# Performance work log

Measured on AMD Instinct MI355X. Metric: run time of the kernel, lower is better.

## Reference

```python
import jax, jax.numpy as jnp
import numpy as np

SCALE_FACTOR = 1.0
VIS_MAX = 1024


def setup_inputs() -> dict:
    key = jax.random.key(0)
    kq, kk, kv = jax.random.split(key, 3)
    B, C, H, W = 4, 256, 64, 64
    Q = jax.random.normal(kq, (B, C, H, W), dtype=jnp.float32)
    K = jax.random.normal(kk, (B, C, H, W), dtype=jnp.float32)
    V = jax.random.normal(kv, (B, C, H, W), dtype=jnp.float32)
    return {"Q": Q, "K": K, "V": V}


def reference(Q, K, V):
    # Q,K: [B,C,H,W] -> flatten spatial dims to HW
    B, C, H, W = Q.shape
    HW = H * W
    Q_flat = Q.reshape(B, C, HW).transpose(0, 2, 1)  # [B, HW, C]
    K_flat = K.reshape(B, C, HW)                      # [B, C, HW]
    # Full scaled score matrix [B, HW, HW]; argmax over keys reproduces the
    # chunked running-max/argmax (strict '>' update keeps first max, matching
    # jnp.argmax tie-breaking).
    S = jnp.einsum('bqc,bck->bqk', Q_flat, K_flat) * SCALE_FACTOR
    H_idx = jnp.argmax(S, axis=2).astype(jnp.int64)   # [B, HW]
    vis = min(VIS_MAX, HW)
    S_vis = S[:, :vis, :vis]                          # [B, vis, vis]
    return S_vis, H_idx
```

## Files before the change

### kernel.cpp

```cpp
#include <hip/hip_runtime.h>
#include <stdint.h>

#define B_   4
#define C_   256
#define HW_  4096
#define VIS_ 1024
#define KE_  768

using half8   = __attribute__((ext_vector_type(8))) _Float16;
using floatx4 = __attribute__((ext_vector_type(4))) float;

__device__ __forceinline__ unsigned mapf(float v) {
    unsigned u = __float_as_uint(v);
    return (u & 0x80000000u) ? ~u : (u | 0x80000000u);
}

__global__ void init_ws_kernel(unsigned long long* ws, int n) {
    int i = blockIdx.x * blockDim.x + threadIdx.x;
    if (i < n) ws[i] = 0ull;
}

__global__ void finalize_kernel(const unsigned long long* __restrict__ ws,
                                float* __restrict__ out1, int n) {
    int i = blockIdx.x * blockDim.x + threadIdx.x;
    if (i < n) {
        unsigned kinv = (unsigned)(ws[i] & 0xFFFFFFFFull);
        out1[i] = (float)(HW_ - 1 - (int)kinv);
    }
}


__global__ __launch_bounds__(256) void split_transpose_kernel(
    const float* __restrict__ Q, const float* __restrict__ K,
    _Float16* __restrict__ Aexp, _Float16* __restrict__ Bexp)
{
    __shared__ float tile[64][65];
    const int hw0 = blockIdx.x * 64;
    const int c0  = blockIdx.y * 64;
    const int z = blockIdx.z, b = z >> 1, which = z & 1;
    const float* src = (which ? K : Q) + (size_t)b * C_ * HW_;
    _Float16* dst = (which ? Bexp : Aexp) + (size_t)b * HW_ * KE_;
    const int t = threadIdx.x;

    #pragma unroll
    for (int i = 0; i < 4; ++i) {
        int c  = (t >> 4) + i * 16;
        int hw = (t & 15) * 4;
        float4 v = *(const float4*)(src + (size_t)(c0 + c) * HW_ + hw0 + hw);
        tile[c][hw] = v.x; tile[c][hw+1] = v.y; tile[c][hw+2] = v.z; tile[c][hw+3] = v.w;
    }
    __syncthreads();

    #pragma unroll
    for (int i = 0; i < 2; ++i) {
        int id  = t + i * 256;
        int row = id >> 3;
        int c8  = (id & 7) * 8;
        half8 h8, l8;
        #pragma unroll
        for (int j = 0; j < 8; ++j) {
            float v = tile[c8 + j][row];
            _Float16 h = (_Float16)v;
            h8[j] = h;
            l8[j] = (_Float16)(v - (float)h);
        }
        _Float16* base = dst + (size_t)(hw0 + row) * KE_ + c0 + c8;
        *(half8*)(base + 0 * C_) = h8;
        *(half8*)(base + 1 * C_) = which ? l8 : h8;
        *(half8*)(base + 2 * C_) = which ? h8 : l8;
    }
}

__device__ __forceinline__ void gl2lds16(const _Float16* g, _Float16* l) {
    __builtin_amdgcn_global_load_lds(
        (const __attribute__((address_space(1))) void*)g,
        (__attribute__((address_space(3))) void*)l, 16, 0, 0);
}

__global__ __launch_bounds__(256, 2) void gemm_mfma_kernel(
    const _Float16* __restrict__ Aexp, const _Float16* __restrict__ Bexp,
    float* __restrict__ out0, unsigned long long* __restrict__ keys)
{
    __shared__ __align__(16) _Float16 Al[128 * 32];
    __shared__ __align__(16) _Float16 Bl[128 * 32];
    __shared__ unsigned long long red2[128][2];

    const int t    = threadIdx.x;
    const int lane = t & 63;
    const int wave = t >> 6;
    const int quad = lane >> 4;
    const int s    = lane & 15;
    const int wm   = (wave >> 1) * 64;
    const int wn   = (wave & 1) * 64;
    const int kt = blockIdx.x, qt = blockIdx.y, b = blockIdx.z;

    const _Float16* Ab = Aexp + (size_t)b * HW_ * KE_ + (size_t)(qt * 128) * KE_;
    const _Float16* Bb = Bexp + (size_t)b * HW_ * KE_ + (size_t)(kt * 128) * KE_;

    const int ca = t, cb = t + 256;
    const int ra = ca >> 2, oa = (ca & 3) * 8;
    const int rb = cb >> 2, ob = (cb & 3) * 8;

    floatx4 acc[4][4] = {};

    for (int it = 0; it < KE_ / 32; ++it) {
        const int k0 = it * 32;
        gl2lds16(Ab + (size_t)ra * KE_ + k0 + oa, Al + ca * 8);
        gl2lds16(Ab + (size_t)rb * KE_ + k0 + ob, Al + cb * 8);
        gl2lds16(Bb + (size_t)ra * KE_ + k0 + oa, Bl + ca * 8);
        gl2lds16(Bb + (size_t)rb * KE_ + k0 + ob, Bl + cb * 8);
        __syncthreads();

        half8 a[4], bf[4];
        #pragma unroll
        for (int mi = 0; mi < 4; ++mi)
            a[mi] = *(half8*)(Al + (wm + mi * 16 + s) * 32 + quad * 8);
        #pragma unroll
        for (int ni = 0; ni < 4; ++ni)
            bf[ni] = *(half8*)(Bl + (wn + ni * 16 + s) * 32 + quad * 8);
        #pragma unroll
        for (int mi = 0; mi < 4; ++mi)
            #pragma unroll
            for (int ni = 0; ni < 4; ++ni)
                acc[mi][ni] = __builtin_amdgcn_mfma_f32_16x16x32_f16(a[mi], bf[ni], acc[mi][ni], 0, 0, 0);
        __syncthreads();
    }

    if (qt < 8 && kt < 8) {
        #pragma unroll
        for (int mi = 0; mi < 4; ++mi)
            #pragma unroll
            for (int r = 0; r < 4; ++r) {
                int grow = qt * 128 + wm + mi * 16 + quad * 4 + r;
                float* orow = out0 + ((size_t)b * VIS_ + grow) * VIS_ + kt * 128;
                #pragma unroll
                for (int ni = 0; ni < 4; ++ni)
                    orow[wn + ni * 16 + s] = acc[mi][ni][r];
            }
    }

    #pragma unroll
    for (int mi = 0; mi < 4; ++mi) {
        #pragma unroll
        for (int r = 0; r < 4; ++r) {
            float best = acc[mi][0][r];
            int bcol = wn + s;
            #pragma unroll
            for (int ni = 1; ni < 4; ++ni) {
                float v = acc[mi][ni][r];
                if (v > best) { best = v; bcol = wn + ni * 16 + s; }
            }
            int gcol = kt * 128 + bcol;
            unsigned long long key = ((unsigned long long)mapf(best) << 32)
                                   | (unsigned)(HW_ - 1 - gcol);
            #pragma unroll
            for (int m = 1; m < 16; m <<= 1) {
                unsigned long long o = __shfl_xor(key, m, 64);
                if (o > key) key = o;
            }
            if (s == 0) red2[wm + mi * 16 + quad * 4 + r][wave & 1] = key;
        }
    }
    __syncthreads();
    if (t < 128) {
        unsigned long long k0v = red2[t][0], k1v = red2[t][1];
        unsigned long long kk = k0v > k1v ? k0v : k1v;
        atomicMax(&keys[(size_t)b * HW_ + qt * 128 + t], kk);
    }
}

#define BT   64
#define BK   32
#define LDP  68

__global__ __launch_bounds__(256) void gemm_argmax_kernel(
    const float* __restrict__ Q, const float* __restrict__ K,
    float* __restrict__ out0, unsigned long long* __restrict__ ws)
{
    __shared__ float As[BK][LDP];
    __shared__ float Bs[BK][LDP];
    __shared__ unsigned long long red[BT][17];

    const int t  = threadIdx.x;
    const int tx = t & 15;
    const int ty = t >> 4;
    const int k0 = blockIdx.x * BT;
    const int q0 = blockIdx.y * BT;
    const int b  = blockIdx.z;

    const float* Qb = Q + (size_t)b * C_ * HW_;
    const float* Kb = K + (size_t)b * C_ * HW_;

    float acc[4][4] = {{0.f},{0.f},{0.f},{0.f}};

    for (int c0 = 0; c0 < C_; c0 += BK) {
        #pragma unroll
        for (int i = 0; i < 2; ++i) {
            int idx = i * 256 + t;
            int row = idx >> 4;
            int col = (idx & 15) * 4;
            const float4 a  = *(const float4*)(Qb + (size_t)(c0 + row) * HW_ + q0 + col);
            const float4 bv = *(const float4*)(Kb + (size_t)(c0 + row) * HW_ + k0 + col);
            *(float4*)(&As[row][col]) = a;
            *(float4*)(&Bs[row][col]) = bv;
        }
        __syncthreads();
        #pragma unroll
        for (int cc = 0; cc < BK; ++cc) {
            const float4 av = *(const float4*)(&As[cc][ty * 4]);
            const float4 bv = *(const float4*)(&Bs[cc][tx * 4]);
            const float a_[4] = {av.x, av.y, av.z, av.w};
            const float b_[4] = {bv.x, bv.y, bv.z, bv.w};
            #pragma unroll
            for (int i = 0; i < 4; ++i)
                #pragma unroll
                for (int j = 0; j < 4; ++j)
                    acc[i][j] = fmaf(a_[i], b_[j], acc[i][j]);
        }
        __syncthreads();
    }

    if (q0 < VIS_ && k0 < VIS_) {
        #pragma unroll
        for (int i = 0; i < 4; ++i) {
            float4 v = make_float4(acc[i][0], acc[i][1], acc[i][2], acc[i][3]);
            size_t off = (size_t)b * VIS_ * VIS_ + (size_t)(q0 + ty * 4 + i) * VIS_ + (k0 + tx * 4);
            *(float4*)(out0 + off) = v;
        }
    }

    #pragma unroll
    for (int i = 0; i < 4; ++i) {
        float best = acc[i][0];
        int   bj   = 0;
        #pragma unroll
        for (int j = 1; j < 4; ++j)
            if (acc[i][j] > best) { best = acc[i][j]; bj = j; }
        int kidx = k0 + tx * 4 + bj;
        unsigned long long key = ((unsigned long long)mapf(best) << 32)
                               | (unsigned)(HW_ - 1 - kidx);
        red[ty * 4 + i][tx] = key;
    }
    __syncthreads();
    if (t < BT) {
        unsigned long long best = red[t][0];
        #pragma unroll
        for (int j = 1; j < 16; ++j) {
            unsigned long long v = red[t][j];
            if (v > best) best = v;
        }
        atomicMax(&ws[(size_t)b * HW_ + q0 + t], best);
    }
}

extern "C" void kernel_launch(void* const* d_in, const int* in_sizes, int n_in,
                              void* d_out, int out_size, void* d_ws, size_t ws_size,
                              hipStream_t stream) {
    const float* Q = (const float*)d_in[0];
    const float* K = (const float*)d_in[1];
    float* out0 = (float*)d_out;
    float* out1 = out0 + (size_t)B_ * VIS_ * VIS_;

    unsigned long long* keys = (unsigned long long*)d_ws;
    const size_t keys_bytes = (size_t)B_ * HW_ * 8;
    const size_t exp_elems  = (size_t)B_ * HW_ * KE_;
    const size_t need = keys_bytes + 2 * exp_elems * sizeof(_Float16);

    const int n = B_ * HW_;
    init_ws_kernel<<<(n + 255) / 256, 256, 0, stream>>>(keys, n);

    if (ws_size >= need) {
        _Float16* Aexp = (_Float16*)((char*)d_ws + keys_bytes);
        _Float16* Bexp = Aexp + exp_elems;
        split_transpose_kernel<<<dim3(HW_ / 64, C_ / 64, 2 * B_), 256, 0, stream>>>(Q, K, Aexp, Bexp);
        gemm_mfma_kernel<<<dim3(HW_ / 128, HW_ / 128, B_), 256, 0, stream>>>(Aexp, Bexp, out0, keys);
    } else {
        gemm_argmax_kernel<<<dim3(HW_ / BT, HW_ / BT, B_), 256, 0, stream>>>(Q, K, out0, keys);
    }

    finalize_kernel<<<(n + 255) / 256, 256, 0, stream>>>(keys, out1, n);
}
```

Before: 233.8 us.

## Switch to 32x32x16 MFMA, dedupe hi/lo split storage, fuse key init

The GEMM now issues 32x32x16 f16 MFMAs on a 2x2 accumulator tile per wave instead of 16x16x32 on a 4x4 tile. The split-precision buffers store hi and lo halves once (512 instead of 768 columns), and the three-phase K loop picks hi/lo offsets by phase. This cuts workspace writes and footprint, and the larger MFMA needs fewer LDS reads per FLOP. The separate zero-init kernel is folded into the transpose kernel, saving one launch. The output and argmax epilogue are remapped to the 32x32 accumulator layout, which risks indexing mistakes.

```diff
diff --git a/kernel.cpp b/kernel.cpp
--- a/kernel.cpp
+++ b/kernel.cpp
@@ -5,10 +5,10 @@
 #define C_   256
 #define HW_  4096
 #define VIS_ 1024
-#define KE_  768
-
-using half8   = __attribute__((ext_vector_type(8))) _Float16;
-using floatx4 = __attribute__((ext_vector_type(4))) float;
+#define KS_  512
+
+using half8    = __attribute__((ext_vector_type(8))) _Float16;
+using floatx16 = __attribute__((ext_vector_type(16))) float;
 
 __device__ __forceinline__ unsigned mapf(float v) {
     unsigned u = __float_as_uint(v);
@@ -32,15 +32,19 @@
 
 __global__ __launch_bounds__(256) void split_transpose_kernel(
     const float* __restrict__ Q, const float* __restrict__ K,
-    _Float16* __restrict__ Aexp, _Float16* __restrict__ Bexp)
+    _Float16* __restrict__ Aexp, _Float16* __restrict__ Bexp,
+    unsigned long long* __restrict__ keys)
 {
     __shared__ float tile[64][65];
     const int hw0 = blockIdx.x * 64;
     const int c0  = blockIdx.y * 64;
     const int z = blockIdx.z, b = z >> 1, which = z & 1;
     const float* src = (which ? K : Q) + (size_t)b * C_ * HW_;
-    _Float16* dst = (which ? Bexp : Aexp) + (size_t)b * HW_ * KE_;
+    _Float16* dst = (which ? Bexp : Aexp) + (size_t)b * HW_ * KS_;
     const int t = threadIdx.x;
+
+    if (blockIdx.y == 0 && blockIdx.z == 0)
+        keys[blockIdx.x * 256 + t] = 0ull;
 
     #pragma unroll
     for (int i = 0; i < 4; ++i) {
@@ -64,10 +68,9 @@
             h8[j] = h;
             l8[j] = (_Float16)(v - (float)h);
         }
-        _Float16* base = dst + (size_t)(hw0 + row) * KE_ + c0 + c8;
-        *(half8*)(base + 0 * C_) = h8;
-        *(half8*)(base + 1 * C_) = which ? l8 : h8;
-        *(half8*)(base + 2 * C_) = which ? h8 : l8;
+        _Float16* base = dst + (size_t)(hw0 + row) * KS_ + c0 + c8;
+        *(half8*)(base)       = h8;
+        *(half8*)(base + 256) = l8;
     }
 }
 
@@ -88,77 +91,83 @@
     const int t    = threadIdx.x;
     const int lane = t & 63;
     const int wave = t >> 6;
-    const int quad = lane >> 4;
-    const int s    = lane & 15;
+    const int l31  = lane & 31;
+    const int g    = lane >> 5;
     const int wm   = (wave >> 1) * 64;
     const int wn   = (wave & 1) * 64;
     const int kt = blockIdx.x, qt = blockIdx.y, b = blockIdx.z;
 
-    const _Float16* Ab = Aexp + (size_t)b * HW_ * KE_ + (size_t)(qt * 128) * KE_;
-    const _Float16* Bb = Bexp + (size_t)b * HW_ * KE_ + (size_t)(kt * 128) * KE_;
+    const _Float16* Ab = Aexp + (size_t)b * HW_ * KS_ + (size_t)(qt * 128) * KS_;
+    const _Float16* Bb = Bexp + (size_t)b * HW_ * KS_ + (size_t)(kt * 128) * KS_;
 
     const int ca = t, cb = t + 256;
     const int ra = ca >> 2, oa = (ca & 3) * 8;
     const int rb = cb >> 2, ob = (cb & 3) * 8;
 
-    floatx4 acc[4][4] = {};
-
-    for (int it = 0; it < KE_ / 32; ++it) {
-        const int k0 = it * 32;
-        gl2lds16(Ab + (size_t)ra * KE_ + k0 + oa, Al + ca * 8);
-        gl2lds16(Ab + (size_t)rb * KE_ + k0 + ob, Al + cb * 8);
-        gl2lds16(Bb + (size_t)ra * KE_ + k0 + oa, Bl + ca * 8);
-        gl2lds16(Bb + (size_t)rb * KE_ + k0 + ob, Bl + cb * 8);
-        __syncthreads();
-
-        half8 a[4], bf[4];
-        #pragma unroll
-        for (int mi = 0; mi < 4; ++mi)
-            a[mi] = *(half8*)(Al + (wm + mi * 16 + s) * 32 + quad * 8);
-        #pragma unroll
-        for (int ni = 0; ni < 4; ++ni)
-            bf[ni] = *(half8*)(Bl + (wn + ni * 16 + s) * 32 + quad * 8);
-        #pragma unroll
-        for (int mi = 0; mi < 4; ++mi)
-            #pragma unroll
-            for (int ni = 0; ni < 4; ++ni)
-                acc[mi][ni] = __builtin_amdgcn_mfma_f32_16x16x32_f16(a[mi], bf[ni], acc[mi][ni], 0, 0, 0);
+    floatx16 acc[2][2] = {};
+
+    for (int it = 0; it < 24; ++it) {
+        const int ph = it >> 3;
+        const int kk = (it & 7) * 32;
+        const _Float16* As_ = Ab + ((ph == 2) ? 256 : 0) + kk;
+        const _Float16* Bs_ = Bb + ((ph == 1) ? 256 : 0) + kk;
+        gl2lds16(As_ + (size_t)ra * KS_ + oa, Al + ca * 8);
+        gl2lds16(As_ + (size_t)rb * KS_ + ob, Al + cb * 8);
+        gl2lds16(Bs_ + (size_t)ra * KS_ + oa, Bl + ca * 8);
+        gl2lds16(Bs_ + (size_t)rb * KS_ + ob, Bl + cb * 8);
+        __syncthreads();
+
+        half8 a[2][2], bf[2][2];
+        #pragma unroll
+        for (int s = 0; s < 2; ++s) {
+            #pragma unroll
+            for (int mi = 0; mi < 2; ++mi)
+                a[s][mi] = *(half8*)(Al + (wm + mi * 32 + l31) * 32 + s * 16 + g * 8);
+            #pragma unroll
+            for (int ni = 0; ni < 2; ++ni)
+                bf[s][ni] = *(half8*)(Bl + (wn + ni * 32 + l31) * 32 + s * 16 + g * 8);
+        }
+        #pragma unroll
+        for (int s = 0; s < 2; ++s)
+            #pragma unroll
+            for (int mi = 0; mi < 2; ++mi)
+                #pragma unroll
+                for (int ni = 0; ni < 2; ++ni)
+                    acc[mi][ni] = __builtin_amdgcn_mfma_f32_32x32x16_f16(
+                        a[s][mi], bf[s][ni], acc[mi][ni], 0, 0, 0);
         __syncthreads();
     }
 
     if (qt < 8 && kt < 8) {
         #pragma unroll
-        for (int mi = 0; mi < 4; ++mi)
-            #pragma unroll
-            for (int r = 0; r < 4; ++r) {
-                int grow = qt * 128 + wm + mi * 16 + quad * 4 + r;
-                float* orow = out0 + ((size_t)b * VIS_ + grow) * VIS_ + kt * 128;
-                #pragma unroll
-                for (int ni = 0; ni < 4; ++ni)
-                    orow[wn + ni * 16 + s] = acc[mi][ni][r];
+        for (int mi = 0; mi < 2; ++mi)
+            #pragma unroll
+            for (int r = 0; r < 16; ++r) {
+                int grow = qt * 128 + wm + mi * 32 + (r & 3) + 8 * (r >> 2) + 4 * g;
+                float* orow = out0 + ((size_t)b * VIS_ + grow) * VIS_ + kt * 128 + wn;
+                orow[l31]      = acc[mi][0][r];
+                orow[32 + l31] = acc[mi][1][r];
             }
     }
 
     #pragma unroll
-    for (int mi = 0; mi < 4; ++mi) {
-        #pragma unroll
-        for (int r = 0; r < 4; ++r) {
-            float best = acc[mi][0][r];
-            int bcol = wn + s;
-            #pragma unroll
-            for (int ni = 1; ni < 4; ++ni) {
-                float v = acc[mi][ni][r];
-                if (v > best) { best = v; bcol = wn + ni * 16 + s; }
-            }
+    for (int mi = 0; mi < 2; ++mi) {
+        #pragma unroll
+        for (int r = 0; r < 16; ++r) {
+            int rloc = wm + mi * 32 + (r & 3) + 8 * (r >> 2) + 4 * g;
+            float v0 = acc[mi][0][r], v1 = acc[mi][1][r];
+            float best = v0;
+            int bcol = wn + l31;
+            if (v1 > best) { best = v1; bcol = wn + 32 + l31; }
             int gcol = kt * 128 + bcol;
             unsigned long long key = ((unsigned long long)mapf(best) << 32)
                                    | (unsigned)(HW_ - 1 - gcol);
             #pragma unroll
-            for (int m = 1; m < 16; m <<= 1) {
+            for (int m = 1; m < 32; m <<= 1) {
                 unsigned long long o = __shfl_xor(key, m, 64);
                 if (o > key) key = o;
             }
-            if (s == 0) red2[wm + mi * 16 + quad * 4 + r][wave & 1] = key;
+            if (l31 == 0) red2[rloc][wave & 1] = key;
         }
     }
     __syncthreads();
@@ -263,18 +272,17 @@
 
     unsigned long long* keys = (unsigned long long*)d_ws;
     const size_t keys_bytes = (size_t)B_ * HW_ * 8;
-    const size_t exp_elems  = (size_t)B_ * HW_ * KE_;
+    const size_t exp_elems  = (size_t)B_ * HW_ * KS_;
     const size_t need = keys_bytes + 2 * exp_elems * sizeof(_Float16);
-
     const int n = B_ * HW_;
-    init_ws_kernel<<<(n + 255) / 256, 256, 0, stream>>>(keys, n);
 
     if (ws_size >= need) {
         _Float16* Aexp = (_Float16*)((char*)d_ws + keys_bytes);
         _Float16* Bexp = Aexp + exp_elems;
-        split_transpose_kernel<<<dim3(HW_ / 64, C_ / 64, 2 * B_), 256, 0, stream>>>(Q, K, Aexp, Bexp);
+        split_transpose_kernel<<<dim3(HW_ / 64, C_ / 64, 2 * B_), 256, 0, stream>>>(Q, K, Aexp, Bexp, keys);
         gemm_mfma_kernel<<<dim3(HW_ / 128, HW_ / 128, B_), 256, 0, stream>>>(Aexp, Bexp, out0, keys);
     } else {
+        init_ws_kernel<<<(n + 255) / 256, 256, 0, stream>>>(keys, n);
         gemm_argmax_kernel<<<dim3(HW_ / BT, HW_ / BT, B_), 256, 0, stream>>>(Q, K, out0, keys);
     }
 
```

After: 282.9 us. 1.21x slower.
